# Kernel tuning notes

Measured on AMD Instinct MI355X. Metric: run time of the kernel, lower is better.

## Reference

```python
import jax, jax.numpy as jnp
import numpy as np
import math

V, D, L, H, T, B = 32000, 1024, 4, 16, 2048, 1
HD = D // H
EPS = 1e-5

def _pos_encoding(T, D):
    pos = jnp.arange(T, dtype=jnp.float32)[:, None]                      # [T,1]
    div = jnp.exp(jnp.arange(0, D, 2, dtype=jnp.float32) * (-math.log(10000.0) / D))
    ang = pos * div                                                      # [T,D/2]
    pe = jnp.zeros((T, D), dtype=jnp.float32)
    pe = pe.at[:, 0::2].set(jnp.sin(ang)).at[:, 1::2].set(jnp.cos(ang))
    return pe

def _layernorm(x, g, b):
    mu = jnp.mean(x, axis=-1, keepdims=True)
    var = jnp.mean(jnp.square(x - mu), axis=-1, keepdims=True)
    return (x - mu) * jax.lax.rsqrt(var + EPS) * g + b

def setup_inputs() -> dict:
    key = jax.random.key(0)
    ks = jax.random.split(key, 16)
    s = 0.02
    inp = {
        'idx': jax.random.randint(ks[0], (B, T), 0, V),
        'embed': jax.random.normal(ks[1], (V, D), jnp.float32) * s,
        'Wq': jax.random.normal(ks[2], (L, D, D), jnp.float32) * s,
        'Wk': jax.random.normal(ks[3], (L, D, D), jnp.float32) * s,
        'Wv': jax.random.normal(ks[4], (L, D, D), jnp.float32) * s,
        'Wo': jax.random.normal(ks[5], (L, D, D), jnp.float32) * s,
        'bq': jnp.zeros((L, D), jnp.float32),
        'bk': jnp.zeros((L, D), jnp.float32),
        'bv': jnp.zeros((L, D), jnp.float32),
        'bo': jnp.zeros((L, D), jnp.float32),
        'ln1_g': jnp.ones((L, D), jnp.float32), 'ln1_b': jnp.zeros((L, D), jnp.float32),
        'ln2_g': jnp.ones((L, D), jnp.float32), 'ln2_b': jnp.zeros((L, D), jnp.float32),
        'w1': jax.random.normal(ks[6], (L, D, 4 * D), jnp.float32) * s,
        'b1': jnp.zeros((L, 4 * D), jnp.float32),
        'w2': jax.random.normal(ks[7], (L, 4 * D, D), jnp.float32) * s,
        'b2': jnp.zeros((L, D), jnp.float32),
        'lnf_g': jnp.ones((D,), jnp.float32), 'lnf_b': jnp.zeros((D,), jnp.float32),
        'head_w': jax.random.normal(ks[8], (D, V), jnp.float32) * s,
    }
    return inp

def _forward(idx, embed, Wq, Wk, Wv, Wo, bq, bk, bv, bo,
             ln1_g, ln1_b, ln2_g, ln2_b, w1, b1, w2, b2, lnf_g, lnf_b, head_w):
    Bs, Ts = idx.shape
    x = embed[idx] + _pos_encoding(Ts, embed.shape[1])[None]            # [B,T,D]
    causal = jnp.tril(jnp.ones((Ts, Ts), dtype=bool))                   # [T,T]
    scale = 1.0 / math.sqrt(HD)

    def block(x, p):
        wq, wk, wv, wo, q_b, k_b, v_b, o_b, g1, be1, g2, be2, fw1, fb1, fw2, fb2 = p
        h = _layernorm(x, g1, be1)
        q = (h @ wq + q_b).reshape(Bs, Ts, H, HD)
        k = (h @ wk + k_b).reshape(Bs, Ts, H, HD)
        v = (h @ wv + v_b).reshape(Bs, Ts, H, HD)
        att = jnp.einsum('bthd,bshd->bhts', q, k) * scale               # [B,H,T,T]
        att = jnp.where(causal, att, -jnp.inf)
        att = jax.nn.softmax(att, axis=-1)
        o = jnp.einsum('bhts,bshd->bthd', att, v).reshape(Bs, Ts, -1)
        x = x + (o @ wo + o_b)
        h2 = _layernorm(x, g2, be2)
        ff = jax.nn.gelu(h2 @ fw1 + fb1, approximate=False) @ fw2 + fb2
        x = x + ff
        return x, None

    params = (Wq, Wk, Wv, Wo, bq, bk, bv, bo, ln1_g, ln1_b, ln2_g, ln2_b, w1, b1, w2, b2)
    x, _ = jax.lax.scan(block, x, params)
    x = _layernorm(x, lnf_g, lnf_b)
    return x @ head_w                                                   # [B,T,V]

def reference(idx, embed, Wq, Wk, Wv, Wo, bq, bk, bv, bo,
              ln1_g, ln1_b, ln2_g, ln2_b, w1, b1, w2, b2, lnf_g, lnf_b, head_w):
    return _forward(idx, embed, Wq, Wk, Wv, Wo, bq, bk, bv, bo,
                    ln1_g, ln1_b, ln2_g, ln2_b, w1, b1, w2, b2, lnf_g, lnf_b, head_w)
```

## Files before the change

kernel.cpp:

```cpp
#include <hip/hip_runtime.h>
#include <cstdint>

using u16 = unsigned short;
using u32 = unsigned int;
typedef __bf16  bf16x8 __attribute__((ext_vector_type(8)));
typedef float   f32x4  __attribute__((ext_vector_type(4)));
typedef float   f32x16 __attribute__((ext_vector_type(16)));

__device__ __forceinline__ u16 f2b(float x) {
    u32 u = __builtin_bit_cast(u32, x);
    u = (u + 0x7fffu + ((u >> 16) & 1u)) >> 16;
    return (u16)u;
}

__device__ __forceinline__ f32x4 mfma16(bf16x8 a, bf16x8 b, f32x4 c) {
    return __builtin_amdgcn_mfma_f32_16x16x32_bf16(a, b, c, 0, 0, 0);
}
__device__ __forceinline__ f32x16 mfma32(bf16x8 a, bf16x8 b, f32x16 c) {
    return __builtin_amdgcn_mfma_f32_32x32x16_bf16(a, b, c, 0, 0, 0);
}

__device__ __forceinline__ void gload16(const void* g, void* lds) {
    auto gp = (__attribute__((address_space(1))) void*)(uintptr_t)g;
    auto lp = (__attribute__((address_space(3))) void*)(uintptr_t)lds;
    __builtin_amdgcn_global_load_lds(gp, lp, 16, 0, 0);
}

__device__ __forceinline__ int2 swz_bmbn(int nbm) {
    const int nwg = gridDim.x, orig = blockIdx.x;
    const int q = nwg >> 3, r = nwg & 7;
    const int xcd = orig & 7, lin = orig >> 3;
    const int id = (xcd < r ? xcd * (q + 1) : r * (q + 1) + (xcd - r) * q) + lin;
    return make_int2(id % nbm, id / nbm);
}

template <int EPI>
__device__ __forceinline__ void gemm128(
    const u16* __restrict__ A, const u16* __restrict__ Bt,
    const float* __restrict__ bias,
    float* __restrict__ outf, u16* __restrict__ outb,
    int M, int N, int K, int bm, int bn)
{
    __shared__ u16 lsA[2][128 * 32];
    __shared__ u16 lsB[2][128 * 32];
    const int tid  = threadIdx.x;
    const int w    = tid >> 6, lane = tid & 63;
    const int lr   = lane & 15, lg = lane >> 4;
    const int m0   = bm * 128, n0 = bn * 128;
    const int wr   = (w >> 1) * 64, wc = (w & 1) * 64;
    f32x4 acc[4][4] = {};

    const int row0 = tid >> 2;
    const int ksw8 = ((lane & 3) ^ ((lane >> 3) & 3)) * 8;
    const u16* a0  = A  + (size_t)(m0 + row0) * K + ksw8;
    const u16* a1  = a0 + (size_t)64 * K;
    const u16* b0p = Bt + (size_t)(n0 + row0) * K + ksw8;
    const u16* b1p = b0p + (size_t)64 * K;
    const int rsw  = (lg ^ ((lr >> 1) & 3)) * 8;

    auto stage = [&](int buf, int ko) {
        char* la = (char*)lsA[buf] + w * 1024;
        char* lb = (char*)lsB[buf] + w * 1024;
        gload16(a0 + ko, la);
        gload16(a1 + ko, la + 4096);
        gload16(b0p + ko, lb);
        gload16(b1p + ko, lb + 4096);
    };
    auto compute = [&](int buf) {
        bf16x8 af[4], bfv[4];
#pragma unroll
        for (int i = 0; i < 4; i++)
            af[i] = *(const bf16x8*)&lsA[buf][(wr + i * 16 + lr) * 32 + rsw];
#pragma unroll
        for (int j = 0; j < 4; j++)
            bfv[j] = *(const bf16x8*)&lsB[buf][(wc + j * 16 + lr) * 32 + rsw];
#pragma unroll
        for (int i = 0; i < 4; i++)
#pragma unroll
            for (int j = 0; j < 4; j++)
                acc[i][j] = mfma16(af[i], bfv[j], acc[i][j]);
    };

    const int nk = K >> 5;
    stage(0, 0);
    __syncthreads();
    int cur = 0;
    for (int kt = 0; kt < nk - 1; ++kt) {
        stage(cur ^ 1, (kt + 1) * 32);
        compute(cur);
        __syncthreads();
        cur ^= 1;
    }
    compute(cur);

#pragma unroll
    for (int j = 0; j < 4; j++) {
        const int gc = n0 + wc + j * 16 + lr;
        float bv = 0.f;
        if constexpr (EPI == 1) bv = bias[gc];
#pragma unroll
        for (int i = 0; i < 4; i++) {
            const int grb = m0 + wr + i * 16 + lg * 4;
#pragma unroll
            for (int r = 0; r < 4; r++) {
                float v = acc[i][j][r] + bv;
                if constexpr (EPI == 1) v = 0.5f * v * (1.f + erff(v * 0.70710678118654752f));
                const size_t o = (size_t)(grb + r) * N + gc;
                if constexpr (EPI == 3) outf[o] = v;
                else                    outb[o] = f2b(v);
            }
        }
    }
}

template <int EPI>
__device__ __forceinline__ void gemm64(
    const u16* __restrict__ A, int lda, const u16* __restrict__ Bt, int ldb,
    const float* __restrict__ bias,
    float* __restrict__ outf, u16* __restrict__ outb,
    int M, int N, int kc, int bm, int bn)
{
    __shared__ u16 lsA[2][64 * 32];
    __shared__ u16 lsB[2][128 * 32];
    const int tid  = threadIdx.x;
    const int w    = tid >> 6, lane = tid & 63;
    const int lr   = lane & 15, lg = lane >> 4;
    const int m0   = bm * 64, n0 = bn * 128;
    const int wc   = w * 32;
    f32x4 acc[4][2] = {};

    const int row0 = tid >> 2;
    const int ksw8 = ((lane & 3) ^ ((lane >> 3) & 3)) * 8;
    const u16* a0  = A  + (size_t)(m0 + row0) * lda + ksw8;
    const u16* b0p = Bt + (size_t)(n0 + row0) * ldb + ksw8;
    const u16* b1p = b0p + (size_t)64 * ldb;
    const int rsw  = (lg ^ ((lr >> 1) & 3)) * 8;

    auto stage = [&](int buf, int ko) {
        char* la = (char*)lsA[buf] + w * 1024;
        char* lb = (char*)lsB[buf] + w * 1024;
        gload16(a0 + ko, la);
        gload16(b0p + ko, lb);
        gload16(b1p + ko, lb + 4096);
    };
    auto compute = [&](int buf) {
        bf16x8 af[4], bfv[2];
#pragma unroll
        for (int i = 0; i < 4; i++)
            af[i] = *(const bf16x8*)&lsA[buf][(i * 16 + lr) * 32 + rsw];
#pragma unroll
        for (int j = 0; j < 2; j++)
            bfv[j] = *(const bf16x8*)&lsB[buf][(wc + j * 16 + lr) * 32 + rsw];
#pragma unroll
        for (int i = 0; i < 4; i++)
#pragma unroll
            for (int j = 0; j < 2; j++)
                acc[i][j] = mfma16(af[i], bfv[j], acc[i][j]);
    };

    const int nk = kc >> 5;
    stage(0, 0);
    __syncthreads();
    int cur = 0;
    for (int kt = 0; kt < nk - 1; ++kt) {
        stage(cur ^ 1, (kt + 1) * 32);
        compute(cur);
        __syncthreads();
        cur ^= 1;
    }
    compute(cur);

#pragma unroll
    for (int j = 0; j < 2; j++) {
        const int gc = n0 + wc + j * 16 + lr;
        float bv = 0.f;
        if constexpr (EPI == 0) bv = bias[gc];
#pragma unroll
        for (int i = 0; i < 4; i++) {
            const int grb = m0 + i * 16 + lg * 4;
#pragma unroll
            for (int r = 0; r < 4; r++) {
                float v = acc[i][j][r] + bv;
                const size_t o = (size_t)(grb + r) * N + gc;
                if constexpr (EPI == 4) outf[o] = v;
                else                    outb[o] = f2b(v);
            }
        }
    }
}

__global__ __launch_bounds__(256) void gemm64_bias_k(
    const u16* A, const u16* Bt, const float* bias, u16* out, int M, int N, int K, int nbm)
{
    int2 b = swz_bmbn(nbm);
    gemm64<0>(A, K, Bt, K, bias, nullptr, out, M, N, K, b.x, b.y);
}
__global__ __launch_bounds__(256) void gemm64_splitk_k(
    const u16* A, const u16* Bt, float* pbuf, int M, int N, int K, int kc, int nbm)
{
    int2 b = swz_bmbn(nbm);
    const int s = blockIdx.y;
    gemm64<4>(A + (size_t)s * kc, K, Bt + (size_t)s * kc, K, nullptr,
              pbuf + (size_t)s * M * N, nullptr, M, N, kc, b.x, b.y);
}
__global__ __launch_bounds__(256) void gemm128_gelu_k(
    const u16* A, const u16* Bt, const float* bias, u16* out, int M, int N, int K, int nbm)
{
    int2 b = swz_bmbn(nbm);
    gemm128<1>(A, Bt, bias, nullptr, out, M, N, K, b.x, b.y);
}
__global__ __launch_bounds__(256) void gemm128_plain_k(
    const u16* A, const u16* Bt, float* out, int M, int N, int K, int nbm)
{
    int2 b = swz_bmbn(nbm);
    gemm128<3>(A, Bt, nullptr, out, nullptr, M, N, K, b.x, b.y);
}

__global__ __launch_bounds__(256) void reduce_ln_k(
    const float* __restrict__ pbuf, int S,
    const float* __restrict__ bias,
    float* __restrict__ x,
    const float* __restrict__ g, const float* __restrict__ bln,
    u16* __restrict__ hb)
{
    __shared__ float red[8];
    const int row = blockIdx.x, tid = threadIdx.x;
    const int w = tid >> 6, lane = tid & 63;
    const size_t base = (size_t)row * 256 + tid;
    float4 v = ((const float4*)x)[base];
    for (int s = 0; s < S; ++s) {
        const float4 p = ((const float4*)pbuf)[(size_t)s * 524288 + base];
        v.x += p.x; v.y += p.y; v.z += p.z; v.w += p.w;
    }
    const float4 bb = ((const float4*)bias)[tid];
    v.x += bb.x; v.y += bb.y; v.z += bb.z; v.w += bb.w;
    ((float4*)x)[base] = v;

    float s1 = v.x + v.y + v.z + v.w;
#pragma unroll
    for (int d = 1; d < 64; d <<= 1) s1 += __shfl_xor(s1, d);
    if (lane == 0) red[w] = s1;
    __syncthreads();
    const float mu = (red[0] + red[1] + red[2] + red[3]) * (1.f / 1024.f);
    const float d0 = v.x - mu, d1 = v.y - mu, d2 = v.z - mu, d3 = v.w - mu;
    float s2 = d0 * d0 + d1 * d1 + d2 * d2 + d3 * d3;
#pragma unroll
    for (int d = 1; d < 64; d <<= 1) s2 += __shfl_xor(s2, d);
    if (lane == 0) red[4 + w] = s2;
    __syncthreads();
    const float var = (red[4] + red[5] + red[6] + red[7]) * (1.f / 1024.f);
    const float rs = rsqrtf(var + 1e-5f);
    const float4 gv = ((const float4*)g)[tid];
    const float4 bv = ((const float4*)bln)[tid];
    u32 p0 = (u32)f2b(d0 * rs * gv.x + bv.x) | ((u32)f2b(d1 * rs * gv.y + bv.y) << 16);
    u32 p1 = (u32)f2b(d2 * rs * gv.z + bv.z) | ((u32)f2b(d3 * rs * gv.w + bv.w) << 16);
    ((uint2*)(hb + (size_t)row * 1024))[tid] = make_uint2(p0, p1);
}

__global__ __launch_bounds__(256) void flash_attn_k(
    const u16* __restrict__ qkv, const u16* __restrict__ vT, u16* __restrict__ out)
{
    constexpr int DS = 3072, T = 2048;
    __shared__ float mrg[2][64][32];
    __shared__ float msh[2][32], lsh[2][32];
    __shared__ u16   sbuf[2][32 * 68];
    const int w = threadIdx.x >> 6, lane = threadIdx.x & 63;
    const int lq = lane & 31, hi = lane >> 5;
    const int hoff = blockIdx.y * 64;
    const int pair = w >> 1, par = w & 1;
    const int qt = (pair == 0) ? blockIdx.x : 63 - blockIdx.x;
    const int q0 = qt * 32;
    const int qg = q0 + lq;

    const u16* qp = qkv + (size_t)qg * DS + hoff;
    const u16* kp = qkv + 1024 + hoff;

    bf16x8 qf[4];
#pragma unroll
    for (int d = 0; d < 4; d++)
        qf[d] = *(const bf16x8*)(qp + d * 16 + hi * 8);

    f32x16 o0 = {}, o1 = {};
    float m_r = -1e30f, l_r = 0.f;

    const int ntiles = (qt >> 1) + 1;
    for (int t = par; t < ntiles; t += 2) {
        const int kv0 = t * 64;
        f32x16 s0 = {}, s1 = {};
        {
            const u16* kb0 = kp + (size_t)(kv0 + lq) * DS + hi * 8;
            const u16* kb1 = kb0 + (size_t)32 * DS;
#pragma unroll
            for (int d = 0; d < 4; d++) {
                s0 = mfma32(*(const bf16x8*)(kb0 + d * 16), qf[d], s0);
                s1 = mfma32(*(const bf16x8*)(kb1 + d * 16), qf[d], s1);
            }
        }
        float p[32];
        float mx = -1e30f;
#pragma unroll
        for (int r = 0; r < 16; r++) {
            const int kvl = (r & 3) + 8 * (r >> 2) + 4 * hi;
            float v0 = (kv0 + kvl      <= qg) ? s0[r] * 0.125f : -1e30f;
            float v1 = (kv0 + 32 + kvl <= qg) ? s1[r] * 0.125f : -1e30f;
            p[r] = v0; p[16 + r] = v1;
            mx = fmaxf(mx, fmaxf(v0, v1));
        }
        mx = fmaxf(mx, __shfl_xor(mx, 32));
        const float mn = fmaxf(m_r, mx);
        const float alpha = __expf(m_r - mn);
        m_r = mn;
        float ls = 0.f;
#pragma unroll
        for (int i = 0; i < 32; i++) { p[i] = __expf(p[i] - mn); ls += p[i]; }
        ls += __shfl_xor(ls, 32);
        l_r = l_r * alpha + ls;
#pragma unroll
        for (int r = 0; r < 16; r++) { o0[r] *= alpha; o1[r] *= alpha; }
#pragma unroll
        for (int sub = 0; sub < 2; sub++) {
            u32 pw[8], x[8];
#pragma unroll
            for (int i = 0; i < 8; i++)
                pw[i] = (u32)f2b(p[sub * 16 + 2 * i]) | ((u32)f2b(p[sub * 16 + 2 * i + 1]) << 16);
#pragma unroll
            for (int i = 0; i < 8; i++) x[i] = __shfl_xor(pw[i], 32);
            u32 b0[4], b1[4];
            b0[0] = hi ? x[2]  : pw[0];  b0[1] = hi ? x[3]  : pw[1];
            b0[2] = hi ? pw[2] : x[0];   b0[3] = hi ? pw[3] : x[1];
            b1[0] = hi ? x[6]  : pw[4];  b1[1] = hi ? x[7]  : pw[5];
            b1[2] = hi ? pw[6] : x[4];   b1[3] = hi ? pw[7] : x[5];
            bf16x8 B0 = __builtin_bit_cast(bf16x8, *(const uint4*)b0);
            bf16x8 B1 = __builtin_bit_cast(bf16x8, *(const uint4*)b1);
            const u16* vb = vT + (size_t)(hoff + lq) * T + kv0 + sub * 32 + hi * 8;
            o0 = mfma32(*(const bf16x8*)vb, B0, o0);
            o0 = mfma32(*(const bf16x8*)(vb + 16), B1, o0);
            const u16* vb1 = vb + (size_t)32 * T;
            o1 = mfma32(*(const bf16x8*)vb1, B0, o1);
            o1 = mfma32(*(const bf16x8*)(vb1 + 16), B1, o1);
        }
    }

    __syncthreads();
    if (par == 0) {
#pragma unroll
        for (int r = 0; r < 16; r++) {
            const int d = (r & 3) + 8 * (r >> 2) + 4 * hi;
            mrg[pair][d][lq]      = o0[r];
            mrg[pair][d + 32][lq] = o1[r];
        }
        if (hi == 0) { msh[pair][lq] = m_r; lsh[pair][lq] = l_r; }
    }
    __syncthreads();
    if (par == 1) {
        const float m0v = msh[pair][lq], l0v = lsh[pair][lq];
        const float M = fmaxf(m0v, m_r);
        const float f0 = __expf(m0v - M), f1 = __expf(m_r - M);
        const float linv = 1.f / (l0v * f0 + l_r * f1);
        u32* sb = (u32*)sbuf[pair];
#pragma unroll
        for (int r = 0; r < 16; r += 2) {
            const int d = (r & 3) + 8 * (r >> 2) + 4 * hi;
            float va = (mrg[pair][d][lq] * f0 + o0[r] * f1) * linv;
            float vb = (mrg[pair][d + 1][lq] * f0 + o0[r + 1] * f1) * linv;
            sb[lq * 34 + (d >> 1)] = (u32)f2b(va) | ((u32)f2b(vb) << 16);
            float vc = (mrg[pair][d + 32][lq] * f0 + o1[r] * f1) * linv;
            float vd = (mrg[pair][d + 33][lq] * f0 + o1[r + 1] * f1) * linv;
            sb[lq * 34 + ((d + 32) >> 1)] = (u32)f2b(vc) | ((u32)f2b(vd) << 16);
        }
#pragma unroll
        for (int ps = 0; ps < 8; ps++) {
            const int row = ps * 4 + (lane >> 4);
            const uint2 v = *(const uint2*)&sbuf[pair][row * 68 + (lane & 15) * 4];
            *(uint2*)(out + (size_t)(q0 + row) * 1024 + hoff + (lane & 15) * 4) = v;
        }
    }
}

__global__ __launch_bounds__(256) void transpose_cvt_k(
    const float* __restrict__ src, u16* __restrict__ dst, int K, int N,
    long long srcLS, long long dstLS)
{
    __shared__ float tile[32][33];
    src += (size_t)blockIdx.z * srcLS;
    dst += (size_t)blockIdx.z * dstLS;
    const int n0 = blockIdx.x * 32, k0 = blockIdx.y * 32;
    const int tx = threadIdx.x & 31, ty = threadIdx.x >> 5;
#pragma unroll
    for (int r = 0; r < 32; r += 8)
        tile[ty + r][tx] = src[(size_t)(k0 + ty + r) * N + n0 + tx];
    __syncthreads();
#pragma unroll
    for (int r = 0; r < 32; r += 8)
        dst[(size_t)(n0 + ty + r) * K + k0 + tx] = f2b(tile[tx][ty + r]);
}

__global__ __launch_bounds__(256) void transpose_u16_k(
    const u16* __restrict__ src, u16* __restrict__ dst, int R, int C, int srcStride)
{
    __shared__ u16 tile[32][33];
    const int c0 = blockIdx.x * 32, r0 = blockIdx.y * 32;
    const int tx = threadIdx.x & 31, ty = threadIdx.x >> 5;
#pragma unroll
    for (int r = 0; r < 32; r += 8)
        tile[ty + r][tx] = src[(size_t)(r0 + ty + r) * srcStride + c0 + tx];
    __syncthreads();
#pragma unroll
    for (int r = 0; r < 32; r += 8)
        dst[(size_t)(c0 + ty + r) * R + r0 + tx] = tile[tx][ty + r];
}

__global__ __launch_bounds__(256) void concat_bias_k(
    const float* __restrict__ bq, const float* __restrict__ bk,
    const float* __restrict__ bv, float* __restrict__ bcat)
{
    const int l = blockIdx.y;
    const int j = blockIdx.x * 256 + threadIdx.x;
    float v;
    if (j < 1024)      v = bq[l * 1024 + j];
    else if (j < 2048) v = bk[l * 1024 + j - 1024];
    else               v = bv[l * 1024 + j - 2048];
    bcat[l * 3072 + j] = v;
}

__global__ __launch_bounds__(256) void embed_pos_k(
    const int* __restrict__ idx, const float* __restrict__ emb, float* __restrict__ x)
{
    const int t = blockIdx.x, tid = threadIdx.x;
    const int tok = idx[t];
    float4 e = ((const float4*)(emb + (size_t)tok * 1024))[tid];
    const int d0 = tid * 4;
    const float c = -0.0089944730195080f;
    const float a0 = (float)t * expf((float)d0 * c);
    const float a1 = (float)t * expf((float)(d0 + 2) * c);
    e.x += sinf(a0); e.y += cosf(a0); e.z += sinf(a1); e.w += cosf(a1);
    ((float4*)(x + (size_t)t * 1024))[tid] = e;
}

__global__ __launch_bounds__(256) void layernorm_k(
    const float* __restrict__ x, const float* __restrict__ g,
    const float* __restrict__ b, u16* __restrict__ out)
{
    __shared__ float red[8];
    const int row = blockIdx.x, tid = threadIdx.x;
    const int w = tid >> 6, lane = tid & 63;
    const float4 v = ((const float4*)(x + (size_t)row * 1024))[tid];
    float s = v.x + v.y + v.z + v.w;
#pragma unroll
    for (int d = 1; d < 64; d <<= 1) s += __shfl_xor(s, d);
    if (lane == 0) red[w] = s;
    __syncthreads();
    const float mu = (red[0] + red[1] + red[2] + red[3]) * (1.f / 1024.f);
    const float d0 = v.x - mu, d1 = v.y - mu, d2 = v.z - mu, d3 = v.w - mu;
    float s2 = d0 * d0 + d1 * d1 + d2 * d2 + d3 * d3;
#pragma unroll
    for (int d = 1; d < 64; d <<= 1) s2 += __shfl_xor(s2, d);
    if (lane == 0) red[4 + w] = s2;
    __syncthreads();
    const float var = (red[4] + red[5] + red[6] + red[7]) * (1.f / 1024.f);
    const float rs = rsqrtf(var + 1e-5f);
    const float4 gv = ((const float4*)g)[tid];
    const float4 bv = ((const float4*)b)[tid];
    u32 p0 = (u32)f2b(d0 * rs * gv.x + bv.x) | ((u32)f2b(d1 * rs * gv.y + bv.y) << 16);
    u32 p1 = (u32)f2b(d2 * rs * gv.z + bv.z) | ((u32)f2b(d3 * rs * gv.w + bv.w) << 16);
    ((uint2*)(out + (size_t)row * 1024))[tid] = make_uint2(p0, p1);
}

extern "C" void kernel_launch(void* const* d_in, const int* in_sizes, int n_in,
                              void* d_out, int out_size, void* d_ws, size_t ws_size,
                              hipStream_t stream)
{
    const int*   idx   = (const int*)  d_in[0];
    const float* embed = (const float*)d_in[1];
    const float* Wq    = (const float*)d_in[2];
    const float* Wk    = (const float*)d_in[3];
    const float* Wv    = (const float*)d_in[4];
    const float* Wo    = (const float*)d_in[5];
    const float* bq    = (const float*)d_in[6];
    const float* bk    = (const float*)d_in[7];
    const float* bv    = (const float*)d_in[8];
    const float* bo    = (const float*)d_in[9];
    const float* ln1g  = (const float*)d_in[10];
    const float* ln1b  = (const float*)d_in[11];
    const float* ln2g  = (const float*)d_in[12];
    const float* ln2b  = (const float*)d_in[13];
    const float* w1    = (const float*)d_in[14];
    const float* b1    = (const float*)d_in[15];
    const float* w2    = (const float*)d_in[16];
    const float* b2    = (const float*)d_in[17];
    const float* lnfg  = (const float*)d_in[18];
    const float* lnfb  = (const float*)d_in[19];
    const float* headw = (const float*)d_in[20];

    char* ws = (char*)d_ws;
    auto alloc = [&](size_t bytes) {
        char* p = ws;
        ws += (bytes + 255) & ~(size_t)255;
        return p;
    };
    u16*   qkvT = (u16*)alloc((size_t)4 * 3072 * 1024 * 2);
    u16*   WoT  = (u16*)alloc((size_t)4 * 1024 * 1024 * 2);
    u16*   w1T  = (u16*)alloc((size_t)4 * 1024 * 4096 * 2);
    u16*   w2T  = (u16*)alloc((size_t)4 * 1024 * 4096 * 2);
    u16*   hT   = (u16*)alloc((size_t)32000 * 1024 * 2);
    float* bcat = (float*)alloc((size_t)4 * 3072 * 4);
    float* x    = (float*)alloc((size_t)2048 * 1024 * 4);
    u16*   hb   = (u16*)alloc((size_t)2048 * 1024 * 2);
    u16*   qkvb = (u16*)alloc((size_t)2048 * 3072 * 2);
    u16*   vTb  = (u16*)alloc((size_t)2048 * 1024 * 2);
    u16*   ab   = (u16*)alloc((size_t)2048 * 1024 * 2);
    u16*   ff   = (u16*)alloc((size_t)2048 * 4096 * 2);
    float* pbuf = (float*)d_out;

    transpose_cvt_k<<<dim3(32, 32, 4),  256, 0, stream>>>(Wq, qkvT,            1024, 1024, 1048576, 3145728);
    transpose_cvt_k<<<dim3(32, 32, 4),  256, 0, stream>>>(Wk, qkvT + 1048576,  1024, 1024, 1048576, 3145728);
    transpose_cvt_k<<<dim3(32, 32, 4),  256, 0, stream>>>(Wv, qkvT + 2097152,  1024, 1024, 1048576, 3145728);
    transpose_cvt_k<<<dim3(32, 32, 4),  256, 0, stream>>>(Wo, WoT,             1024, 1024, 1048576, 1048576);
    transpose_cvt_k<<<dim3(128, 32, 4), 256, 0, stream>>>(w1, w1T,             1024, 4096, 4194304, 4194304);
    transpose_cvt_k<<<dim3(32, 128, 4), 256, 0, stream>>>(w2, w2T,             4096, 1024, 4194304, 4194304);
    transpose_cvt_k<<<dim3(1000, 32, 1), 256, 0, stream>>>(headw, hT,          1024, 32000, 0, 0);
    concat_bias_k<<<dim3(12, 4), 256, 0, stream>>>(bq, bk, bv, bcat);

    embed_pos_k<<<dim3(2048), 256, 0, stream>>>(idx, embed, x);
    layernorm_k<<<dim3(2048), 256, 0, stream>>>(x, ln1g, ln1b, hb);

    for (int l = 0; l < 4; ++l) {
        gemm64_bias_k<<<dim3(768), 256, 0, stream>>>(hb, qkvT + (size_t)l * 3145728,
                                                     bcat + l * 3072, qkvb, 2048, 3072, 1024, 32);
        transpose_u16_k<<<dim3(32, 64), 256, 0, stream>>>(qkvb + 2048, vTb, 2048, 1024, 3072);
        flash_attn_k<<<dim3(32, 16), 256, 0, stream>>>(qkvb, vTb, ab);
        gemm64_splitk_k<<<dim3(256, 2), 256, 0, stream>>>(ab, WoT + (size_t)l * 1048576,
                                                          pbuf, 2048, 1024, 1024, 512, 32);
        reduce_ln_k<<<dim3(2048), 256, 0, stream>>>(pbuf, 2, bo + l * 1024, x,
                                                    ln2g + l * 1024, ln2b + l * 1024, hb);
        gemm128_gelu_k<<<dim3(512), 256, 0, stream>>>(hb, w1T + (size_t)l * 4194304,
                                                      b1 + l * 4096, ff, 2048, 4096, 1024, 16);
        gemm64_splitk_k<<<dim3(256, 4), 256, 0, stream>>>(ff, w2T + (size_t)l * 4194304,
                                                          pbuf, 2048, 1024, 4096, 1024, 32);
        const float* ng = (l < 3) ? (ln1g + (l + 1) * 1024) : lnfg;
        const float* nb = (l < 3) ? (ln1b + (l + 1) * 1024) : lnfb;
        reduce_ln_k<<<dim3(2048), 256, 0, stream>>>(pbuf, 4, b2 + l * 1024, x, ng, nb, hb);
    }
    gemm128_plain_k<<<dim3(4000), 256, 0, stream>>>(hb, hT, (float*)d_out, 2048, 32000, 1024, 16);
}
```

Measured before the change: 1.089 ms.

## Add 256x256 multi-stage pipelined GEMM kernel for the LM head projection

Replaces the 128x128 double-buffered head GEMM with a dedicated 512-thread kernel using 256x256 tiles. It keeps a 4-stage LDS ring filled by direct global-to-LDS loads, with explicit vmcnt waits and XOR-swizzled LDS layout, and raises wave priority around the MFMA block. The larger tiles raise arithmetic intensity and the deeper pipeline hides memory latency on the largest GEMM (2048x32000x1024). The cost is about 128KB of LDS per block, limiting occupancy to one block per CU, plus heavier register pressure. It also removes the now-unused fp32 epilogue path from the generic 128 kernel.

After: 1.060 ms. 1.03x faster.

```diff
diff --git a/kernel.cpp b/kernel.cpp
--- a/kernel.cpp
+++ b/kernel.cpp
@@ -32,6 +32,90 @@
     const int xcd = orig & 7, lin = orig >> 3;
     const int id = (xcd < r ? xcd * (q + 1) : r * (q + 1) + (xcd - r) * q) + lin;
     return make_int2(id % nbm, id / nbm);
+}
+
+__global__ __launch_bounds__(512, 2) void gemm256_head_k(
+    const u16* __restrict__ A, const u16* __restrict__ Bt,
+    float* __restrict__ out, int M, int N, int K)
+{
+    __shared__ __align__(16) u16 lsA[4][256 * 32];
+    __shared__ __align__(16) u16 lsB[4][256 * 32];
+    const int nbm = M >> 8;
+    const int2 bb = swz_bmbn(nbm);
+    const int m0 = bb.x * 256, n0 = bb.y * 256;
+    const int tid = threadIdx.x;
+    const int w = tid >> 6, lane = tid & 63;
+    const int wr = (w >> 2) * 128, wc = (w & 3) * 64;
+    const int lr = lane & 15, lg = lane >> 4;
+    const int rsw = (lg ^ ((lr >> 1) & 3)) * 8;
+
+    const int trow = tid >> 2;
+    const int ksw8 = ((tid & 3) ^ ((tid >> 3) & 3)) * 8;
+    const u16* aA = A  + (size_t)(m0 + trow) * K + ksw8;
+    const u16* aB = Bt + (size_t)(n0 + trow) * K + ksw8;
+    u16* dA = &lsA[0][0] + trow * 32 + (tid & 3) * 8;
+    u16* dB = &lsB[0][0] + trow * 32 + (tid & 3) * 8;
+
+    f32x4 acc[8][4] = {};
+
+    auto stage = [&](int h) {
+        const int s = h & 3;
+        const int koff = h * 32;
+        gload16(aA + koff,                 dA + s * 8192);
+        gload16(aA + koff + (size_t)128 * K, dA + s * 8192 + 4096);
+        gload16(aB + koff,                 dB + s * 8192);
+        gload16(aB + koff + (size_t)128 * K, dB + s * 8192 + 4096);
+    };
+
+    const int H = K >> 5;
+    stage(0); stage(1); stage(2);
+    asm volatile("s_waitcnt vmcnt(8)" ::: "memory");
+    __builtin_amdgcn_s_barrier();
+
+    for (int h = 0; h < H; ++h) {
+        __builtin_amdgcn_sched_barrier(0);
+        if (h + 3 < H) stage(h + 3);
+        __builtin_amdgcn_sched_barrier(0);
+        const int rem = H - 1 - h;
+        if (rem >= 3)      asm volatile("s_waitcnt vmcnt(12)" ::: "memory");
+        else if (rem == 2) asm volatile("s_waitcnt vmcnt(8)"  ::: "memory");
+        else if (rem == 1) asm volatile("s_waitcnt vmcnt(4)"  ::: "memory");
+        else               asm volatile("s_waitcnt vmcnt(0)"  ::: "memory");
+        __builtin_amdgcn_s_barrier();
+        __builtin_amdgcn_sched_barrier(0);
+
+        const int s = h & 3;
+        bf16x8 af[8], bfv[4];
+#pragma unroll
+        for (int m = 0; m < 8; m++)
+            af[m] = *(const bf16x8*)&lsA[s][(wr + m * 16 + lr) * 32 + rsw];
+#pragma unroll
+        for (int n = 0; n < 4; n++)
+            bfv[n] = *(const bf16x8*)&lsB[s][(wc + n * 16 + lr) * 32 + rsw];
+
+        __builtin_amdgcn_s_setprio(1);
+#pragma unroll
+        for (int m = 0; m < 8; m++)
+#pragma unroll
+            for (int n = 0; n < 4; n++)
+                acc[m][n] = mfma16(af[m], bfv[n], acc[m][n]);
+        __builtin_amdgcn_s_setprio(0);
+
+        __builtin_amdgcn_sched_barrier(0);
+        __builtin_amdgcn_s_barrier();
+    }
+
+#pragma unroll
+    for (int m = 0; m < 8; m++) {
+        const int gr = m0 + wr + m * 16 + lg * 4;
+#pragma unroll
+        for (int r = 0; r < 4; r++) {
+            float* orow = out + (size_t)(gr + r) * N + n0 + wc + lr;
+#pragma unroll
+            for (int n = 0; n < 4; n++)
+                orow[n * 16] = acc[m][n][r];
+        }
+    }
 }
 
 template <int EPI>
@@ -96,8 +180,7 @@
 #pragma unroll
     for (int j = 0; j < 4; j++) {
         const int gc = n0 + wc + j * 16 + lr;
-        float bv = 0.f;
-        if constexpr (EPI == 1) bv = bias[gc];
+        const float bv = bias[gc];
 #pragma unroll
         for (int i = 0; i < 4; i++) {
             const int grb = m0 + wr + i * 16 + lg * 4;
@@ -105,9 +188,7 @@
             for (int r = 0; r < 4; r++) {
                 float v = acc[i][j][r] + bv;
                 if constexpr (EPI == 1) v = 0.5f * v * (1.f + erff(v * 0.70710678118654752f));
-                const size_t o = (size_t)(grb + r) * N + gc;
-                if constexpr (EPI == 3) outf[o] = v;
-                else                    outb[o] = f2b(v);
+                outb[(size_t)(grb + r) * N + gc] = f2b(v);
             }
         }
     }
@@ -208,12 +289,6 @@
 {
     int2 b = swz_bmbn(nbm);
     gemm128<1>(A, Bt, bias, nullptr, out, M, N, K, b.x, b.y);
-}
-__global__ __launch_bounds__(256) void gemm128_plain_k(
-    const u16* A, const u16* Bt, float* out, int M, int N, int K, int nbm)
-{
-    int2 b = swz_bmbn(nbm);
-    gemm128<3>(A, Bt, nullptr, out, nullptr, M, N, K, b.x, b.y);
 }
 
 __global__ __launch_bounds__(256) void reduce_ln_k(
@@ -541,5 +616,5 @@
         const float* nb = (l < 3) ? (ln1b + (l + 1) * 1024) : lnfb;
         reduce_ln_k<<<dim3(2048), 256, 0, stream>>>(pbuf, 4, b2 + l * 1024, x, ng, nb, hb);
     }
-    gemm128_plain_k<<<dim3(4000), 256, 0, stream>>>(hb, hT, (float*)d_out, 2048, 32000, 1024, 16);
-}
+    gemm256_head_k<<<dim3(1000), 512, 0, stream>>>(hb, hT, (float*)d_out, 2048, 32000, 1024);
+}
```

## Replace GEMM kernels with unified deep-pipelined 4-stage LDS GEMM template

Applied to the files above, without the earlier changes.

Replaces the separate 64- and 128-tile double-buffered GEMMs with one templated kernel. It uses a 4-slot LDS ring with loads issued three K-steps ahead, explicit vmcnt waits and a single barrier per step. LDS fragment reads for the next step are interleaved with MFMA groups under setprio, and the QKV and split-K GEMMs move from 64x128 to 128x128 tiles. The LM head uses a 256x256 tile with 512 threads. The change targets load latency, barrier overhead and low data reuse per tile, at the cost of more LDS and registers per block and fewer blocks for the smaller GEMMs.

Measured after the change: 983.4 us. 9.7% less time.

```diff
diff --git a/kernel.cpp b/kernel.cpp
--- a/kernel.cpp
+++ b/kernel.cpp
@@ -34,186 +34,127 @@
     return make_int2(id % nbm, id / nbm);
 }
 
-template <int EPI>
-__device__ __forceinline__ void gemm128(
-    const u16* __restrict__ A, const u16* __restrict__ Bt,
-    const float* __restrict__ bias,
-    float* __restrict__ outf, u16* __restrict__ outb,
-    int M, int N, int K, int bm, int bn)
-{
-    __shared__ u16 lsA[2][128 * 32];
-    __shared__ u16 lsB[2][128 * 32];
-    const int tid  = threadIdx.x;
-    const int w    = tid >> 6, lane = tid & 63;
-    const int lr   = lane & 15, lg = lane >> 4;
-    const int m0   = bm * 128, n0 = bn * 128;
-    const int wr   = (w >> 1) * 64, wc = (w & 1) * 64;
-    f32x4 acc[4][4] = {};
-
-    const int row0 = tid >> 2;
-    const int ksw8 = ((lane & 3) ^ ((lane >> 3) & 3)) * 8;
-    const u16* a0  = A  + (size_t)(m0 + row0) * K + ksw8;
-    const u16* a1  = a0 + (size_t)64 * K;
-    const u16* b0p = Bt + (size_t)(n0 + row0) * K + ksw8;
-    const u16* b1p = b0p + (size_t)64 * K;
-    const int rsw  = (lg ^ ((lr >> 1) & 3)) * 8;
-
-    auto stage = [&](int buf, int ko) {
-        char* la = (char*)lsA[buf] + w * 1024;
-        char* lb = (char*)lsB[buf] + w * 1024;
-        gload16(a0 + ko, la);
-        gload16(a1 + ko, la + 4096);
-        gload16(b0p + ko, lb);
-        gload16(b1p + ko, lb + 4096);
+template <int BM, int KC, int EPI>
+__global__ __launch_bounds__(BM == 256 ? 512 : 256, 2) void gemm_deep_k(
+    const u16* __restrict__ A, int lda, const u16* __restrict__ Bt, int ldb,
+    const float* __restrict__ bias, float* __restrict__ outf,
+    u16* __restrict__ outb, int N, int nbm, int sk, long long sOut)
+{
+    constexpr int NW    = (BM == 256) ? 8 : 4;
+    constexpr int WCOLS = (BM == 256) ? 4 : 2;
+    constexpr int MF    = BM / 32;
+    constexpr int NF    = 4;
+    constexpr int SLOT  = BM * 32;
+    constexpr int HALF  = (BM / 2) * 32;
+    constexpr int H     = KC >> 5;
+    constexpr int RPG   = (MF + NF) / 4;
+    constexpr int MPG   = (MF * NF) / 4;
+
+    __shared__ __align__(16) u16 lsA[4][SLOT];
+    __shared__ __align__(16) u16 lsB[4][SLOT];
+
+    const int s = blockIdx.y;
+    A  += (size_t)s * sk;
+    Bt += (size_t)s * sk;
+    if (EPI == 4) outf += (size_t)s * sOut;
+
+    const int2 bb = swz_bmbn(nbm);
+    const int m0 = bb.x * BM, n0 = bb.y * BM;
+    const int tid = threadIdx.x;
+    const int w = tid >> 6, lane = tid & 63;
+    const int wr = (w / WCOLS) * (MF * 16), wc = (w % WCOLS) * 64;
+    const int lr = lane & 15, lg = lane >> 4;
+    const int rsw = (lg ^ ((lr >> 1) & 3)) * 8;
+
+    const int trow = tid >> 2;
+    const int ksw8 = ((tid & 3) ^ ((tid >> 3) & 3)) * 8;
+    const u16* aA = A  + (size_t)(m0 + trow) * lda + ksw8;
+    const u16* aB = Bt + (size_t)(n0 + trow) * ldb + ksw8;
+    u16* dA = &lsA[0][0] + trow * 32 + (tid & 3) * 8;
+    u16* dB = &lsB[0][0] + trow * 32 + (tid & 3) * 8;
+
+    f32x4 acc[MF][NF] = {};
+
+    auto stage = [&](int h) {
+        const int sl = h & 3;
+        const int koff = h * 32;
+        gload16(aA + koff,                          dA + sl * SLOT);
+        gload16(aA + koff + (size_t)(BM / 2) * lda, dA + sl * SLOT + HALF);
+        gload16(aB + koff,                          dB + sl * SLOT);
+        gload16(aB + koff + (size_t)(BM / 2) * ldb, dB + sl * SLOT + HALF);
     };
-    auto compute = [&](int buf) {
-        bf16x8 af[4], bfv[4];
-#pragma unroll
-        for (int i = 0; i < 4; i++)
-            af[i] = *(const bf16x8*)&lsA[buf][(wr + i * 16 + lr) * 32 + rsw];
-#pragma unroll
-        for (int j = 0; j < 4; j++)
-            bfv[j] = *(const bf16x8*)&lsB[buf][(wc + j * 16 + lr) * 32 + rsw];
-#pragma unroll
-        for (int i = 0; i < 4; i++)
-#pragma unroll
-            for (int j = 0; j < 4; j++)
-                acc[i][j] = mfma16(af[i], bfv[j], acc[i][j]);
+
+    bf16x8 ra0[MF], rb0[NF], ra1[MF], rb1[NF];
+    auto lreadAll = [&](bf16x8* af, bf16x8* bf, int h) {
+        const int sl = h & 3;
+#pragma unroll
+        for (int m = 0; m < MF; m++)
+            af[m] = *(const bf16x8*)&lsA[sl][(wr + m * 16 + lr) * 32 + rsw];
+#pragma unroll
+        for (int n = 0; n < NF; n++)
+            bf[n] = *(const bf16x8*)&lsB[sl][(wc + n * 16 + lr) * 32 + rsw];
     };
 
-    const int nk = K >> 5;
-    stage(0, 0);
-    __syncthreads();
-    int cur = 0;
-    for (int kt = 0; kt < nk - 1; ++kt) {
-        stage(cur ^ 1, (kt + 1) * 32);
-        compute(cur);
-        __syncthreads();
-        cur ^= 1;
-    }
-    compute(cur);
-
-#pragma unroll
-    for (int j = 0; j < 4; j++) {
-        const int gc = n0 + wc + j * 16 + lr;
+    auto body = [&](int h, bf16x8* aC, bf16x8* bC, bf16x8* aN, bf16x8* bN) {
+        if (h + 3 < H) stage(h + 3);
+        __builtin_amdgcn_sched_barrier(0);
+        asm volatile("s_waitcnt lgkmcnt(0)" ::: "memory");
+        const int rem = H - 1 - h;
+        if (rem >= 3)      asm volatile("s_waitcnt vmcnt(8)" ::: "memory");
+        else if (rem == 2) asm volatile("s_waitcnt vmcnt(4)" ::: "memory");
+        else if (rem == 1) asm volatile("s_waitcnt vmcnt(0)" ::: "memory");
+        __builtin_amdgcn_s_barrier();
+        __builtin_amdgcn_sched_barrier(0);
+        const int sl1 = (h + 1) & 3;
+        const bool doRead = (h + 1 < H);
+#pragma unroll
+        for (int g = 0; g < 4; ++g) {
+            if (doRead) {
+#pragma unroll
+                for (int t = g * RPG; t < (g + 1) * RPG; ++t) {
+                    if (t < MF) aN[t]      = *(const bf16x8*)&lsA[sl1][(wr + t * 16 + lr) * 32 + rsw];
+                    else        bN[t - MF] = *(const bf16x8*)&lsB[sl1][(wc + (t - MF) * 16 + lr) * 32 + rsw];
+                }
+            }
+            __builtin_amdgcn_sched_barrier(0);
+            __builtin_amdgcn_s_setprio(1);
+#pragma unroll
+            for (int i = g * MPG; i < (g + 1) * MPG; ++i)
+                acc[i / NF][i % NF] = mfma16(aC[i / NF], bC[i % NF], acc[i / NF][i % NF]);
+            __builtin_amdgcn_s_setprio(0);
+            __builtin_amdgcn_sched_barrier(0);
+        }
+    };
+
+    stage(0); stage(1); stage(2);
+    asm volatile("s_waitcnt vmcnt(8)" ::: "memory");
+    __builtin_amdgcn_s_barrier();
+    lreadAll(ra0, rb0, 0);
+
+#pragma unroll
+    for (int h = 0; h < H; h += 2) {
+        body(h,     ra0, rb0, ra1, rb1);
+        body(h + 1, ra1, rb1, ra0, rb0);
+    }
+
+#pragma unroll
+    for (int n = 0; n < NF; n++) {
+        const int gc = n0 + wc + n * 16 + lr;
         float bv = 0.f;
-        if constexpr (EPI == 1) bv = bias[gc];
-#pragma unroll
-        for (int i = 0; i < 4; i++) {
-            const int grb = m0 + wr + i * 16 + lg * 4;
+        if constexpr (EPI == 0 || EPI == 1) bv = bias[gc];
+#pragma unroll
+        for (int m = 0; m < MF; m++) {
+            const int grb = m0 + wr + m * 16 + lg * 4;
 #pragma unroll
             for (int r = 0; r < 4; r++) {
-                float v = acc[i][j][r] + bv;
+                float v = acc[m][n][r] + bv;
                 if constexpr (EPI == 1) v = 0.5f * v * (1.f + erff(v * 0.70710678118654752f));
                 const size_t o = (size_t)(grb + r) * N + gc;
-                if constexpr (EPI == 3) outf[o] = v;
-                else                    outb[o] = f2b(v);
+                if constexpr (EPI == 3 || EPI == 4) outf[o] = v;
+                else                                outb[o] = f2b(v);
             }
         }
     }
-}
-
-template <int EPI>
-__device__ __forceinline__ void gemm64(
-    const u16* __restrict__ A, int lda, const u16* __restrict__ Bt, int ldb,
-    const float* __restrict__ bias,
-    float* __restrict__ outf, u16* __restrict__ outb,
-    int M, int N, int kc, int bm, int bn)
-{
-    __shared__ u16 lsA[2][64 * 32];
-    __shared__ u16 lsB[2][128 * 32];
-    const int tid  = threadIdx.x;
-    const int w    = tid >> 6, lane = tid & 63;
-    const int lr   = lane & 15, lg = lane >> 4;
-    const int m0   = bm * 64, n0 = bn * 128;
-    const int wc   = w * 32;
-    f32x4 acc[4][2] = {};
-
-    const int row0 = tid >> 2;
-    const int ksw8 = ((lane & 3) ^ ((lane >> 3) & 3)) * 8;
-    const u16* a0  = A  + (size_t)(m0 + row0) * lda + ksw8;
-    const u16* b0p = Bt + (size_t)(n0 + row0) * ldb + ksw8;
-    const u16* b1p = b0p + (size_t)64 * ldb;
-    const int rsw  = (lg ^ ((lr >> 1) & 3)) * 8;
-
-    auto stage = [&](int buf, int ko) {
-        char* la = (char*)lsA[buf] + w * 1024;
-        char* lb = (char*)lsB[buf] + w * 1024;
-        gload16(a0 + ko, la);
-        gload16(b0p + ko, lb);
-        gload16(b1p + ko, lb + 4096);
-    };
-    auto compute = [&](int buf) {
-        bf16x8 af[4], bfv[2];
-#pragma unroll
-        for (int i = 0; i < 4; i++)
-            af[i] = *(const bf16x8*)&lsA[buf][(i * 16 + lr) * 32 + rsw];
-#pragma unroll
-        for (int j = 0; j < 2; j++)
-            bfv[j] = *(const bf16x8*)&lsB[buf][(wc + j * 16 + lr) * 32 + rsw];
-#pragma unroll
-        for (int i = 0; i < 4; i++)
-#pragma unroll
-            for (int j = 0; j < 2; j++)
-                acc[i][j] = mfma16(af[i], bfv[j], acc[i][j]);
-    };
-
-    const int nk = kc >> 5;
-    stage(0, 0);
-    __syncthreads();
-    int cur = 0;
-    for (int kt = 0; kt < nk - 1; ++kt) {
-        stage(cur ^ 1, (kt + 1) * 32);
-        compute(cur);
-        __syncthreads();
-        cur ^= 1;
-    }
-    compute(cur);
-
-#pragma unroll
-    for (int j = 0; j < 2; j++) {
-        const int gc = n0 + wc + j * 16 + lr;
-        float bv = 0.f;
-        if constexpr (EPI == 0) bv = bias[gc];
-#pragma unroll
-        for (int i = 0; i < 4; i++) {
-            const int grb = m0 + i * 16 + lg * 4;
-#pragma unroll
-            for (int r = 0; r < 4; r++) {
-                float v = acc[i][j][r] + bv;
-                const size_t o = (size_t)(grb + r) * N + gc;
-                if constexpr (EPI == 4) outf[o] = v;
-                else                    outb[o] = f2b(v);
-            }
-        }
-    }
-}
-
-__global__ __launch_bounds__(256) void gemm64_bias_k(
-    const u16* A, const u16* Bt, const float* bias, u16* out, int M, int N, int K, int nbm)
-{
-    int2 b = swz_bmbn(nbm);
-    gemm64<0>(A, K, Bt, K, bias, nullptr, out, M, N, K, b.x, b.y);
-}
-__global__ __launch_bounds__(256) void gemm64_splitk_k(
-    const u16* A, const u16* Bt, float* pbuf, int M, int N, int K, int kc, int nbm)
-{
-    int2 b = swz_bmbn(nbm);
-    const int s = blockIdx.y;
-    gemm64<4>(A + (size_t)s * kc, K, Bt + (size_t)s * kc, K, nullptr,
-              pbuf + (size_t)s * M * N, nullptr, M, N, kc, b.x, b.y);
-}
-__global__ __launch_bounds__(256) void gemm128_gelu_k(
-    const u16* A, const u16* Bt, const float* bias, u16* out, int M, int N, int K, int nbm)
-{
-    int2 b = swz_bmbn(nbm);
-    gemm128<1>(A, Bt, bias, nullptr, out, M, N, K, b.x, b.y);
-}
-__global__ __launch_bounds__(256) void gemm128_plain_k(
-    const u16* A, const u16* Bt, float* out, int M, int N, int K, int nbm)
-{
-    int2 b = swz_bmbn(nbm);
-    gemm128<3>(A, Bt, nullptr, out, nullptr, M, N, K, b.x, b.y);
 }
 
 __global__ __launch_bounds__(256) void reduce_ln_k(
@@ -525,21 +466,26 @@
     layernorm_k<<<dim3(2048), 256, 0, stream>>>(x, ln1g, ln1b, hb);
 
     for (int l = 0; l < 4; ++l) {
-        gemm64_bias_k<<<dim3(768), 256, 0, stream>>>(hb, qkvT + (size_t)l * 3145728,
-                                                     bcat + l * 3072, qkvb, 2048, 3072, 1024, 32);
+        gemm_deep_k<128, 1024, 0><<<dim3(384), 256, 0, stream>>>(
+            hb, 1024, qkvT + (size_t)l * 3145728, 1024,
+            bcat + l * 3072, nullptr, qkvb, 3072, 16, 0, 0);
         transpose_u16_k<<<dim3(32, 64), 256, 0, stream>>>(qkvb + 2048, vTb, 2048, 1024, 3072);
         flash_attn_k<<<dim3(32, 16), 256, 0, stream>>>(qkvb, vTb, ab);
-        gemm64_splitk_k<<<dim3(256, 2), 256, 0, stream>>>(ab, WoT + (size_t)l * 1048576,
-                                                          pbuf, 2048, 1024, 1024, 512, 32);
+        gemm_deep_k<128, 512, 4><<<dim3(128, 2), 256, 0, stream>>>(
+            ab, 1024, WoT + (size_t)l * 1048576, 1024,
+            nullptr, pbuf, nullptr, 1024, 16, 512, 2097152);
         reduce_ln_k<<<dim3(2048), 256, 0, stream>>>(pbuf, 2, bo + l * 1024, x,
                                                     ln2g + l * 1024, ln2b + l * 1024, hb);
-        gemm128_gelu_k<<<dim3(512), 256, 0, stream>>>(hb, w1T + (size_t)l * 4194304,
-                                                      b1 + l * 4096, ff, 2048, 4096, 1024, 16);
-        gemm64_splitk_k<<<dim3(256, 4), 256, 0, stream>>>(ff, w2T + (size_t)l * 4194304,
-                                                          pbuf, 2048, 1024, 4096, 1024, 32);
+        gemm_deep_k<128, 1024, 1><<<dim3(512), 256, 0, stream>>>(
+            hb, 1024, w1T + (size_t)l * 4194304, 1024,
+            b1 + l * 4096, nullptr, ff, 4096, 16, 0, 0);
+        gemm_deep_k<128, 1024, 4><<<dim3(128, 4), 256, 0, stream>>>(
+            ff, 4096, w2T + (size_t)l * 4194304, 4096,
+            nullptr, pbuf, nullptr, 1024, 16, 1024, 2097152);
         const float* ng = (l < 3) ? (ln1g + (l + 1) * 1024) : lnfg;
         const float* nb = (l < 3) ? (ln1b + (l + 1) * 1024) : lnfb;
         reduce_ln_k<<<dim3(2048), 256, 0, stream>>>(pbuf, 4, b2 + l * 1024, x, ng, nb, hb);
     }
-    gemm128_plain_k<<<dim3(4000), 256, 0, stream>>>(hb, hT, (float*)d_out, 2048, 32000, 1024, 16);
-}
+    gemm_deep_k<256, 1024, 3><<<dim3(1000), 512, 0, stream>>>(
+        hb, 1024, hT, 1024, nullptr, (float*)d_out, nullptr, 32000, 8, 0, 0);
+}
```
